# Performance work log

Measured on AMD Instinct MI355X. Metric: run time of the kernel, lower is better.

The kernel has to match this reference:

```python
import jax, jax.numpy as jnp
import numpy as np

B, D1, SN, NF = 32, 49, 32, 16          # batch, n_sais, sqrt_n, n_filters
D_MODEL, HEADS = SN * SN * NF, 16        # 16384, 16
DEPTH = D_MODEL // HEADS                 # 1024
C_IN = 16


def setup_inputs() -> dict:
    key = jax.random.key(0)
    ks = jax.random.split(key, 11)
    mk = lambda k, shape, scale=1.0: jax.random.normal(k, shape, dtype=jnp.float32) * scale
    w_scale = 1.0 / np.sqrt(C_IN)
    return {
        "v": mk(ks[0], (B, D1, SN, SN, C_IN)),
        "k": mk(ks[1], (B, D1, SN, SN, C_IN)),
        "q": mk(ks[2], (B, D1, SN, SN, C_IN)),
        # 1x1x1 Conv3D == pointwise channel matmul: weight [C_in, n_filters] + bias
        "Wq": mk(ks[3], (C_IN, NF), w_scale), "bq": jnp.zeros((NF,), jnp.float32),
        "Wk": mk(ks[4], (C_IN, NF), w_scale), "bk": jnp.zeros((NF,), jnp.float32),
        "Wv": mk(ks[5], (C_IN, NF), w_scale), "bv": jnp.zeros((NF,), jnp.float32),
        "Wo": mk(ks[6], (NF, NF), w_scale),   "bo": jnp.zeros((NF,), jnp.float32),
    }


def _pointwise(x, W, b):
    # Conv3D(kernel=1, padding='same') over [B, d1, h, w, c]
    return jnp.einsum('bdhwc,cf->bdhwf', x, W) + b


def reference(v, k, q, Wq, bq, Wk, bk, Wv, bv, Wo, bo):
    b = q.shape[0]
    # projections (1x1x1 conv3d), then flatten spatial+channel into d_model
    def proj_heads(x, W, bias):
        y = _pointwise(x, W, bias).reshape(b, D1, D_MODEL)       # reshape2d
        y = y.reshape(b, D1, HEADS, DEPTH)                        # split_heads
        return y.transpose(0, 2, 1, 3)                            # [b, h, d1, depth]
    qh = proj_heads(q, Wq, bq)
    kh = proj_heads(k, Wk, bk)
    vh = proj_heads(v, Wv, bv)
    # scaled dot-product attention over the 49 SAI tokens
    scale = 1.0 / jnp.sqrt(jnp.float32(DEPTH))
    scores = jnp.einsum('bhqd,bhkd->bhqk', qh, kh) * scale        # [b, h, 49, 49]
    attn = jax.nn.softmax(scores, axis=-1)
    ctx = jnp.einsum('bhqk,bhkd->bhqd', attn, vh)                 # [b, h, 49, depth]
    ctx = ctx.transpose(0, 2, 1, 3).reshape(b, D1, D_MODEL)       # concat heads
    ctx = ctx.reshape(b, D1, SN, SN, NF)                          # reshape4d
    out = _pointwise(ctx, Wo, bo)                                 # wout conv3d 1x1x1
    return out, attn
```

## Files before the change

### kernel.cpp

```cpp
#include <hip/hip_runtime.h>
#include <hip/hip_bf16.h>


#define NT 49
#define TOKS 16384
#define HSL 1024
#define SLOT 3200
#define ZSWZ(n) (((((n) & 7) ^ (((n) >> 3) & 7))) << 4)

typedef __attribute__((ext_vector_type(8))) short bf16x8;
typedef __attribute__((ext_vector_type(4))) float f32x4;

__device__ __forceinline__ ushort f2bf(float f) {
    union { float f; unsigned u; } v; v.f = f;
    return (ushort)((v.u + 0x7fffu + ((v.u >> 16) & 1u)) >> 16);
}
__device__ __forceinline__ unsigned pk2(float f0, float f1) {
    return (unsigned)f2bf(f0) | ((unsigned)f2bf(f1) << 16);
}
__device__ __forceinline__ float4 f4mul(float s, float4 w) {
    return make_float4(s*w.x, s*w.y, s*w.z, s*w.w);
}
__device__ __forceinline__ float4 f4fma(float s, float4 w, float4 a) {
    a.x = fmaf(s, w.x, a.x); a.y = fmaf(s, w.y, a.y);
    a.z = fmaf(s, w.z, a.z); a.w = fmaf(s, w.w, a.w);
    return a;
}
__device__ __forceinline__ float red4s(float v) {
    v += __shfl_xor(v, 1); v += __shfl_xor(v, 2); return v;
}
__device__ __forceinline__ float4 red4v(float4 v) {
    return make_float4(red4s(v.x), red4s(v.y), red4s(v.z), red4s(v.w));
}

#define W_DECL(mb) \
    const float4 W00 = *(const float4*)((mb)+ 0), W01 = *(const float4*)((mb)+ 4), \
                 W02 = *(const float4*)((mb)+ 8), W03 = *(const float4*)((mb)+12), \
                 W10 = *(const float4*)((mb)+16), W11 = *(const float4*)((mb)+20), \
                 W12 = *(const float4*)((mb)+24), W13 = *(const float4*)((mb)+28), \
                 W20 = *(const float4*)((mb)+32), W21 = *(const float4*)((mb)+36), \
                 W22 = *(const float4*)((mb)+40), W23 = *(const float4*)((mb)+44), \
                 W30 = *(const float4*)((mb)+48), W31 = *(const float4*)((mb)+52), \
                 W32 = *(const float4*)((mb)+56), W33 = *(const float4*)((mb)+60)

#define PROJ_BFLY(a, y0, y1, y2, y3) \
    float4 y0 = f4mul((a).x, W00); y0 = f4fma((a).y, W10, y0); \
    y0 = f4fma((a).z, W20, y0);    y0 = f4fma((a).w, W30, y0); \
    float4 y1 = f4mul((a).x, W01); y1 = f4fma((a).y, W11, y1); \
    y1 = f4fma((a).z, W21, y1);    y1 = f4fma((a).w, W31, y1); \
    float4 y2 = f4mul((a).x, W02); y2 = f4fma((a).y, W12, y2); \
    y2 = f4fma((a).z, W22, y2);    y2 = f4fma((a).w, W32, y2); \
    float4 y3 = f4mul((a).x, W03); y3 = f4fma((a).y, W13, y3); \
    y3 = f4fma((a).z, W23, y3);    y3 = f4fma((a).w, W33, y3); \
    y0 = red4v(y0); y1 = red4v(y1); y2 = red4v(y2); y3 = red4v(y3)

template<int SPLIT, int LOG2S>
__global__ __launch_bounds__(256, 2) void k_scores(
    const float* __restrict__ qin, const float* __restrict__ kin,
    const float* __restrict__ Wq, const float* __restrict__ bq,
    const float* __restrict__ Wk, float* __restrict__ ws1)
{
    __shared__ ushort bufA[64*128];
    __shared__ ushort bufB[64*128];
    __shared__ float  Msh[256];
    __shared__ float  wkbqSh[16];
    __shared__ float  gSh[64];

    const int tid  = threadIdx.x;
    const int lane = tid & 63;
    const int wv   = tid >> 6;
    const int s    = blockIdx.x & (SPLIT - 1);
    const int h    = (blockIdx.x >> LOG2S) & 15;
    const int b    = blockIdx.x >> (LOG2S + 4);

    const float* qbase = qin + (size_t)b*NT*TOKS + h*HSL + s*(1024/SPLIT);
    const float* kbase = kin + (size_t)b*NT*TOKS + h*HSL + s*(1024/SPLIT);

    {
        unsigned* z0 = (unsigned*)bufA; unsigned* z1 = (unsigned*)bufB;
        for (int i = tid; i < 4096; i += 256) { z0[i] = 0u; z1[i] = 0u; }
        const int c1 = tid >> 4, c2 = tid & 15;
        float m = 0.f;
        #pragma unroll
        for (int f = 0; f < 16; ++f) m += Wq[c1*16+f] * Wk[c2*16+f];
        Msh[tid] = m;
        if (tid < 16) {
            float wb = 0.f;
            #pragma unroll
            for (int g = 0; g < 16; ++g) wb += Wk[tid*16+g] * bq[g];
            wkbqSh[tid] = wb;
        }
        if (tid < 64) gSh[tid] = 0.f;
    }
    __syncthreads();

    const float* mb = Msh + (lane & 3)*64;
    W_DECL(mb);

    const int f4 = tid & 31;
    const int t0 = tid >> 5;
    const int r  = f4 & 3;

    f32x4 accS[4];
    #pragma unroll
    for (int nt = 0; nt < 4; ++nt) accS[nt] = (f32x4){0.f,0.f,0.f,0.f};

    for (int kc = 0; kc < 8/SPLIT; ++kc) {
        const float* qc = qbase + kc*128 + f4*4;
        const float* kp = kbase + kc*128 + f4*4;
        float4 qv[7], kv[7];
        #pragma unroll
        for (int i = 0; i < 7; ++i) {
            const int t  = t0 + 8*i;
            const int tc = t < 48 ? t : 48;
            qv[i] = *(const float4*)(qc + (size_t)tc*TOKS);
            kv[i] = *(const float4*)(kp + (size_t)tc*TOKS);
        }
        #pragma unroll
        for (int i = 0; i < 7; ++i) {
            const int t = t0 + 8*i;
            if (t >= NT) {
                qv[i] = make_float4(0.f,0.f,0.f,0.f);
                kv[i] = make_float4(0.f,0.f,0.f,0.f);
            }
            PROJ_BFLY(qv[i], y0, y1, y2, y3);
            uint2 w;
            if      (r == 0) { w.x = pk2(y0.x, y0.y); w.y = pk2(y0.z, y0.w); }
            else if (r == 1) { w.x = pk2(y1.x, y1.y); w.y = pk2(y1.z, y1.w); }
            else if (r == 2) { w.x = pk2(y2.x, y2.y); w.y = pk2(y2.z, y2.w); }
            else             { w.x = pk2(y3.x, y3.y); w.y = pk2(y3.z, y3.w); }
            const int addrA = (t*256 + (f4 >> 2)*32 + r*8) ^ ((t & 7) << 4);
            *(uint2*)((char*)bufA + addrA) = w;
            uint2 wk2; wk2.x = pk2(kv[i].x, kv[i].y); wk2.y = pk2(kv[i].z, kv[i].w);
            const int addrB = (t*256 + f4*8) ^ ((t & 7) << 4);
            *(uint2*)((char*)bufB + addrB) = wk2;
            const float* wb = wkbqSh + r*4;
            const float pg = kv[i].x*wb[0] + kv[i].y*wb[1] + kv[i].z*wb[2] + kv[i].w*wb[3];
            if (pg != 0.f) atomicAdd(&gSh[t], pg);
        }
        __syncthreads();
        #pragma unroll
        for (int ks = 0; ks < 4; ++ks) {
            const int ra  = wv*16 + (lane & 15);
            const int abo = (ra*256 + (ks*32 + (lane >> 4)*8)*2) ^ ((ra & 7) << 4);
            const bf16x8 af = *(const bf16x8*)((const char*)bufA + abo);
            #pragma unroll
            for (int nt = 0; nt < 4; ++nt) {
                const int rb  = nt*16 + (lane & 15);
                const int bbo = (rb*256 + (ks*32 + (lane >> 4)*8)*2) ^ ((rb & 7) << 4);
                const bf16x8 bf = *(const bf16x8*)((const char*)bufB + bbo);
                accS[nt] = __builtin_amdgcn_mfma_f32_16x16x32_bf16(af, bf, accS[nt], 0, 0, 0);
            }
        }
        __syncthreads();
    }

    float* slot = ws1 + (size_t)blockIdx.x * SLOT;
    #pragma unroll
    for (int nt = 0; nt < 4; ++nt) {
        const int col = nt*16 + (lane & 15);
        #pragma unroll
        for (int rr = 0; rr < 4; ++rr) {
            const int row = wv*16 + (lane >> 4)*4 + rr;
            if (row < NT) slot[row*64 + col] = accS[nt][rr];
        }
    }
    if (tid < 64) slot[3136 + tid] = gSh[tid];
}

template<int SPLIT>
__global__ __launch_bounds__(256, 2) void k_softmax(
    const float* __restrict__ ws1, float* __restrict__ attnp,
    ushort* __restrict__ ws2)
{
    __shared__ float sS[NT*69];
    __shared__ float sG[64];
    const int tid = threadIdx.x;
    const float* base = ws1 + (size_t)blockIdx.x * SPLIT * SLOT;

    for (int p = tid; p < 784; p += 256) {
        const int row = p >> 4, c4 = (p & 15) * 4;
        float4 acc = *(const float4*)(base + row*64 + c4);
        #pragma unroll
        for (int s = 1; s < SPLIT; ++s) {
            const float4 a = *(const float4*)(base + s*SLOT + row*64 + c4);
            acc.x += a.x; acc.y += a.y; acc.z += a.z; acc.w += a.w;
        }
        sS[row*69 + c4 + 0] = acc.x;
        sS[row*69 + c4 + 1] = acc.y;
        sS[row*69 + c4 + 2] = acc.z;
        sS[row*69 + c4 + 3] = acc.w;
    }
    if (tid < 64) {
        float g = base[3136 + tid];
        #pragma unroll
        for (int s = 1; s < SPLIT; ++s) g += base[s*SLOT + 3136 + tid];
        sG[tid] = g;
    }
    __syncthreads();

    if (tid < NT) {
        float mx = -1e30f;
        for (int j = 0; j < NT; ++j) {
            const float v = (sS[tid*69 + j] + sG[j]) * 0.03125f;
            sS[tid*69 + j] = v;
            mx = fmaxf(mx, v);
        }
        float ssum = 0.f;
        for (int j = 0; j < NT; ++j) {
            const float e = __expf(sS[tid*69 + j] - mx);
            sS[tid*69 + j] = e; ssum += e;
        }
        const float inv = 1.0f / ssum;
        for (int j = 0; j < NT; ++j) sS[tid*69 + j] *= inv;
    }
    __syncthreads();

    float* ab = attnp + (size_t)blockIdx.x * (NT*NT);
    for (int p = tid; p < NT*NT; p += 256) {
        const int t = p / NT, j = p - t*NT;
        ab[p] = sS[t*69 + j];
    }
    ushort* w2 = ws2 + (size_t)blockIdx.x * 4096;
    for (int p = tid; p < 4096; p += 256) {
        const int t = p >> 6, j = p & 63;
        const float v = (t < NT && j < NT) ? sS[t*69 + j] : 0.f;
        w2[p] = f2bf(v);
    }
}

__global__ __launch_bounds__(256, 2) void k_out(
    const float* __restrict__ vin,
    const float* __restrict__ Wv, const float* __restrict__ bv,
    const float* __restrict__ Wo, const float* __restrict__ bo,
    const ushort* __restrict__ ws2, float* __restrict__ out)
{
    __shared__ unsigned Zt[4096];
    __shared__ float WvoSh[256];
    __shared__ float bvoSh[16];

    const int tid  = threadIdx.x;
    const int lane = tid & 63;
    const int wv   = tid >> 6;
    const int kc   = blockIdx.x & 7;
    const int h    = (blockIdx.x >> 3) & 15;
    const int b    = blockIdx.x >> 7;
    const float* vbase = vin + (size_t)b*NT*TOKS + h*HSL;

    {
        const int c1 = tid >> 4, c2 = tid & 15;
        float wvo = 0.f;
        #pragma unroll
        for (int f = 0; f < 16; ++f) wvo += Wv[c1*16+f] * Wo[f*16+c2];
        WvoSh[tid] = wvo;
        if (tid < 16) {
            float s2 = 0.f;
            #pragma unroll
            for (int g = 0; g < 16; ++g) s2 += bv[g]*Wo[g*16+tid];
            bvoSh[tid] = s2 + bo[tid];
        }
        for (int i = tid; i < 1024; i += 256) {
            const int n = i >> 3, pr = 24 + (i & 7);
            if (pr >= 25)
                *(unsigned*)((char*)Zt + ((n*128 + pr*4) ^ ZSWZ(n))) = 0u;
        }
    }
    __syncthreads();

    const ushort* w2 = ws2 + ((size_t)(blockIdx.x >> 3)) * 4096;
    const int ra = wv*16 + (lane & 15);
    const bf16x8 af0 = *(const bf16x8*)(w2 + ra*64 +      (lane >> 4)*8);
    const bf16x8 af1 = *(const bf16x8*)(w2 + ra*64 + 32 + (lane >> 4)*8);

    const float* mb = WvoSh + (lane & 3)*64;
    W_DECL(mb);

    const int f4 = tid & 31;
    const int t0 = tid >> 5;
    const int r  = f4 & 3;

    float4 vv[7];
    {
        const float* vc = vbase + kc*128 + f4*4;
        #pragma unroll
        for (int i = 0; i < 7; ++i) {
            const int t  = t0 + 8*i;
            const int tc = t < 48 ? t : 48;
            vv[i] = *(const float4*)(vc + (size_t)tc*TOKS);
        }
    }
    #pragma unroll
    for (int i = 0; i < 7; ++i) {
        const int t = t0 + 8*i;
        if (t >= NT) vv[i] = make_float4(0.f,0.f,0.f,0.f);
        PROJ_BFLY(vv[i], y0, y1, y2, y3);
        float4 sel;
        if      (r == 0) sel = y0;
        else if (r == 1) sel = y1;
        else if (r == 2) sel = y2;
        else             sel = y3;
        float4 po;
        po.x = __shfl_xor(sel.x, 32); po.y = __shfl_xor(sel.y, 32);
        po.z = __shfl_xor(sel.z, 32); po.w = __shfl_xor(sel.w, 32);
        if (lane < 32) {
            const int n0 = (f4 >> 2)*16 + r*4;
            const int pair = wv + 4*i;
            *(unsigned*)((char*)Zt + (((n0+0)*128 + pair*4) ^ ZSWZ(n0+0))) = pk2(sel.x, po.x);
            *(unsigned*)((char*)Zt + (((n0+1)*128 + pair*4) ^ ZSWZ(n0+1))) = pk2(sel.y, po.y);
            *(unsigned*)((char*)Zt + (((n0+2)*128 + pair*4) ^ ZSWZ(n0+2))) = pk2(sel.z, po.z);
            *(unsigned*)((char*)Zt + (((n0+3)*128 + pair*4) ^ ZSWZ(n0+3))) = pk2(sel.w, po.w);
        }
    }
    __syncthreads();

    float* obase = out + (size_t)b*NT*TOKS + h*HSL + kc*128;
    #pragma unroll
    for (int nt2 = 0; nt2 < 8; ++nt2) {
        const int n    = nt2*16 + (lane & 15);
        const int swzn = ZSWZ(n);
        const bf16x8 bf0 = *(const bf16x8*)((const char*)Zt + ((n*128 +      (lane >> 4)*16) ^ swzn));
        const bf16x8 bf1 = *(const bf16x8*)((const char*)Zt + ((n*128 + 64 + (lane >> 4)*16) ^ swzn));
        f32x4 acc = (f32x4){0.f, 0.f, 0.f, 0.f};
        acc = __builtin_amdgcn_mfma_f32_16x16x32_bf16(af0, bf0, acc, 0, 0, 0);
        acc = __builtin_amdgcn_mfma_f32_16x16x32_bf16(af1, bf1, acc, 0, 0, 0);
        const float bias = bvoSh[n & 15];
        #pragma unroll
        for (int r2 = 0; r2 < 4; ++r2) {
            const int row = wv*16 + (lane >> 4)*4 + r2;
            if (row < NT) obase[(size_t)row*TOKS + n] = acc[r2] + bias;
        }
    }
}

extern "C" void kernel_launch(void* const* d_in, const int* in_sizes, int n_in,
                              void* d_out, int out_size, void* d_ws, size_t ws_size,
                              hipStream_t stream) {
    const float* v  = (const float*)d_in[0];
    const float* k  = (const float*)d_in[1];
    const float* q  = (const float*)d_in[2];
    const float* Wq = (const float*)d_in[3];
    const float* bq = (const float*)d_in[4];
    const float* Wk = (const float*)d_in[5];
    const float* bk = (const float*)d_in[6];
    const float* Wv = (const float*)d_in[7];
    const float* bv = (const float*)d_in[8];
    const float* Wo = (const float*)d_in[9];
    const float* bo = (const float*)d_in[10];
    (void)bk; (void)in_sizes; (void)n_in; (void)out_size;

    float* outp  = (float*)d_out;
    float* attnp = outp + (size_t)32 * 49 * 16384;
    float* ws1   = (float*)d_ws;

    const size_t need4 = (size_t)2048*SLOT*4 + (size_t)512*4096*2;
    if (ws_size >= need4) {
        ushort* ws2 = (ushort*)(ws1 + (size_t)2048*SLOT);
        k_scores<4,2><<<dim3(2048), dim3(256), 0, stream>>>(q, k, Wq, bq, Wk, ws1);
        k_softmax<4> <<<dim3(512),  dim3(256), 0, stream>>>(ws1, attnp, ws2);
        k_out        <<<dim3(4096), dim3(256), 0, stream>>>(v, Wv, bv, Wo, bo, ws2, outp);
    } else {
        ushort* ws2 = (ushort*)(ws1 + (size_t)1024*SLOT);
        k_scores<2,1><<<dim3(1024), dim3(256), 0, stream>>>(q, k, Wq, bq, Wk, ws1);
        k_softmax<2> <<<dim3(512),  dim3(256), 0, stream>>>(ws1, attnp, ws2);
        k_out        <<<dim3(4096), dim3(256), 0, stream>>>(v, Wv, bv, Wo, bo, ws2, outp);
    }
}
```

Baseline: 152.5 us.

## Prefetch next q/k chunk into registers, hoist loads, use hardware bf16 pack

The first kernel now issues global loads for the next q/k chunk while the current chunk is projected, stored to LDS and fed to MFMA, so load latency overlaps compute. The first chunk's loads, and in the output kernel the v and ws2 loads, are moved ahead of the shared-memory setup and weight precompute. The software round-to-nearest bf16 packing is replaced by the v_cvt_pk_bf16_f32 instruction. This costs more live registers, which may hurt occupancy under the 2-block launch bounds.

Result: slower. 158.8 us (+4.1%).

```diff
diff --git a/kernel.cpp b/kernel.cpp
--- a/kernel.cpp
+++ b/kernel.cpp
@@ -15,8 +15,10 @@
     union { float f; unsigned u; } v; v.f = f;
     return (ushort)((v.u + 0x7fffu + ((v.u >> 16) & 1u)) >> 16);
 }
-__device__ __forceinline__ unsigned pk2(float f0, float f1) {
-    return (unsigned)f2bf(f0) | ((unsigned)f2bf(f1) << 16);
+__device__ __forceinline__ unsigned pk2(float lo, float hi) {
+    unsigned r;
+    asm("v_cvt_pk_bf16_f32 %0, %1, %2" : "=v"(r) : "v"(lo), "v"(hi));
+    return r;
 }
 __device__ __forceinline__ float4 f4mul(float s, float4 w) {
     return make_float4(s*w.x, s*w.y, s*w.z, s*w.w);
@@ -76,6 +78,23 @@
     const float* qbase = qin + (size_t)b*NT*TOKS + h*HSL + s*(1024/SPLIT);
     const float* kbase = kin + (size_t)b*NT*TOKS + h*HSL + s*(1024/SPLIT);
 
+    const int f4 = tid & 31;
+    const int t0 = tid >> 5;
+    const int r  = f4 & 3;
+
+    float4 qv[7], kv[7];
+    {
+        const float* qc = qbase + f4*4;
+        const float* kp = kbase + f4*4;
+        #pragma unroll
+        for (int i = 0; i < 7; ++i) {
+            const int t  = t0 + 8*i;
+            const int tc = t < 48 ? t : 48;
+            qv[i] = *(const float4*)(qc + (size_t)tc*TOKS);
+            kv[i] = *(const float4*)(kp + (size_t)tc*TOKS);
+        }
+    }
+
     {
         unsigned* z0 = (unsigned*)bufA; unsigned* z1 = (unsigned*)bufB;
         for (int i = tid; i < 4096; i += 256) { z0[i] = 0u; z1[i] = 0u; }
@@ -97,33 +116,28 @@
     const float* mb = Msh + (lane & 3)*64;
     W_DECL(mb);
 
-    const int f4 = tid & 31;
-    const int t0 = tid >> 5;
-    const int r  = f4 & 3;
-
     f32x4 accS[4];
     #pragma unroll
     for (int nt = 0; nt < 4; ++nt) accS[nt] = (f32x4){0.f,0.f,0.f,0.f};
 
-    for (int kc = 0; kc < 8/SPLIT; ++kc) {
-        const float* qc = qbase + kc*128 + f4*4;
-        const float* kp = kbase + kc*128 + f4*4;
-        float4 qv[7], kv[7];
+    constexpr int NC = 8 / SPLIT;
+    for (int kc = 0; kc < NC; ++kc) {
+        const float* qn = qbase + (kc+1)*128 + f4*4;
+        const float* kn = kbase + (kc+1)*128 + f4*4;
         #pragma unroll
         for (int i = 0; i < 7; ++i) {
             const int t  = t0 + 8*i;
             const int tc = t < 48 ? t : 48;
-            qv[i] = *(const float4*)(qc + (size_t)tc*TOKS);
-            kv[i] = *(const float4*)(kp + (size_t)tc*TOKS);
-        }
-        #pragma unroll
-        for (int i = 0; i < 7; ++i) {
-            const int t = t0 + 8*i;
+            float4 xq = qv[i], xk = kv[i];
+            if (kc + 1 < NC) {
+                qv[i] = *(const float4*)(qn + (size_t)tc*TOKS);
+                kv[i] = *(const float4*)(kn + (size_t)tc*TOKS);
+            }
             if (t >= NT) {
-                qv[i] = make_float4(0.f,0.f,0.f,0.f);
-                kv[i] = make_float4(0.f,0.f,0.f,0.f);
+                xq = make_float4(0.f,0.f,0.f,0.f);
+                xk = make_float4(0.f,0.f,0.f,0.f);
             }
-            PROJ_BFLY(qv[i], y0, y1, y2, y3);
+            PROJ_BFLY(xq, y0, y1, y2, y3);
             uint2 w;
             if      (r == 0) { w.x = pk2(y0.x, y0.y); w.y = pk2(y0.z, y0.w); }
             else if (r == 1) { w.x = pk2(y1.x, y1.y); w.y = pk2(y1.z, y1.w); }
@@ -131,11 +145,11 @@
             else             { w.x = pk2(y3.x, y3.y); w.y = pk2(y3.z, y3.w); }
             const int addrA = (t*256 + (f4 >> 2)*32 + r*8) ^ ((t & 7) << 4);
             *(uint2*)((char*)bufA + addrA) = w;
-            uint2 wk2; wk2.x = pk2(kv[i].x, kv[i].y); wk2.y = pk2(kv[i].z, kv[i].w);
+            uint2 wk2; wk2.x = pk2(xk.x, xk.y); wk2.y = pk2(xk.z, xk.w);
             const int addrB = (t*256 + f4*8) ^ ((t & 7) << 4);
             *(uint2*)((char*)bufB + addrB) = wk2;
             const float* wb = wkbqSh + r*4;
-            const float pg = kv[i].x*wb[0] + kv[i].y*wb[1] + kv[i].z*wb[2] + kv[i].w*wb[3];
+            const float pg = xk.x*wb[0] + xk.y*wb[1] + xk.z*wb[2] + xk.w*wb[3];
             if (pg != 0.f) atomicAdd(&gSh[t], pg);
         }
         __syncthreads();
@@ -247,6 +261,25 @@
     const int b    = blockIdx.x >> 7;
     const float* vbase = vin + (size_t)b*NT*TOKS + h*HSL;
 
+    const int f4 = tid & 31;
+    const int t0 = tid >> 5;
+    const int r  = f4 & 3;
+
+    float4 vv[7];
+    {
+        const float* vc = vbase + kc*128 + f4*4;
+        #pragma unroll
+        for (int i = 0; i < 7; ++i) {
+            const int t  = t0 + 8*i;
+            const int tc = t < 48 ? t : 48;
+            vv[i] = *(const float4*)(vc + (size_t)tc*TOKS);
+        }
+    }
+    const ushort* w2 = ws2 + ((size_t)(blockIdx.x >> 3)) * 4096;
+    const int ra = wv*16 + (lane & 15);
+    const bf16x8 af0 = *(const bf16x8*)(w2 + ra*64 +      (lane >> 4)*8);
+    const bf16x8 af1 = *(const bf16x8*)(w2 + ra*64 + 32 + (lane >> 4)*8);
+
     {
         const int c1 = tid >> 4, c2 = tid & 15;
         float wvo = 0.f;
@@ -267,28 +300,9 @@
     }
     __syncthreads();
 
-    const ushort* w2 = ws2 + ((size_t)(blockIdx.x >> 3)) * 4096;
-    const int ra = wv*16 + (lane & 15);
-    const bf16x8 af0 = *(const bf16x8*)(w2 + ra*64 +      (lane >> 4)*8);
-    const bf16x8 af1 = *(const bf16x8*)(w2 + ra*64 + 32 + (lane >> 4)*8);
-
     const float* mb = WvoSh + (lane & 3)*64;
     W_DECL(mb);
 
-    const int f4 = tid & 31;
-    const int t0 = tid >> 5;
-    const int r  = f4 & 3;
-
-    float4 vv[7];
-    {
-        const float* vc = vbase + kc*128 + f4*4;
-        #pragma unroll
-        for (int i = 0; i < 7; ++i) {
-            const int t  = t0 + 8*i;
-            const int tc = t < 48 ? t : 48;
-            vv[i] = *(const float4*)(vc + (size_t)tc*TOKS);
-        }
-    }
     #pragma unroll
     for (int i = 0; i < 7; ++i) {
         const int t = t0 + 8*i;
```

## Rework per-thread projection mapping and add SPLIT=8 scores path

Applied to the files above, without the earlier changes.

Replaces the butterfly-shuffle projection, where each lane multiplies 4 channels and reduces across lanes, with a layout in which each thread loads all 16 channels of one spatial point and computes 4 output filters by direct dot products, removing cross-lane shuffles. Q and V loads are software-pipelined one token ahead, and K loads for the first chunk are issued before the shared-memory setup. A new SPLIT=8 configuration launches 4096 score blocks when the workspace is large enough, at the cost of more partial slots for softmax to reduce. The final barrier in the chunk loop is skipped on the last iteration.

Measured after the change: 131.2 us. -13.9%, faster.

```diff
diff --git a/kernel.cpp b/kernel.cpp
--- a/kernel.cpp
+++ b/kernel.cpp
@@ -15,22 +15,20 @@
     union { float f; unsigned u; } v; v.f = f;
     return (ushort)((v.u + 0x7fffu + ((v.u >> 16) & 1u)) >> 16);
 }
-__device__ __forceinline__ unsigned pk2(float f0, float f1) {
-    return (unsigned)f2bf(f0) | ((unsigned)f2bf(f1) << 16);
-}
-__device__ __forceinline__ float4 f4mul(float s, float4 w) {
-    return make_float4(s*w.x, s*w.y, s*w.z, s*w.w);
-}
-__device__ __forceinline__ float4 f4fma(float s, float4 w, float4 a) {
-    a.x = fmaf(s, w.x, a.x); a.y = fmaf(s, w.y, a.y);
-    a.z = fmaf(s, w.z, a.z); a.w = fmaf(s, w.w, a.w);
-    return a;
-}
-__device__ __forceinline__ float red4s(float v) {
-    v += __shfl_xor(v, 1); v += __shfl_xor(v, 2); return v;
-}
-__device__ __forceinline__ float4 red4v(float4 v) {
-    return make_float4(red4s(v.x), red4s(v.y), red4s(v.z), red4s(v.w));
+__device__ __forceinline__ unsigned pk2(float lo, float hi) {
+    return (unsigned)f2bf(lo) | ((unsigned)f2bf(hi) << 16);
+}
+__device__ __forceinline__ float qdot(float4 x0, float4 x1, float4 x2, float4 x3,
+                                      float4 wa, float4 wb, float4 wc, float4 wd) {
+    float s =      x0.x*wa.x;
+    s = fmaf(x0.y, wa.y, s); s = fmaf(x0.z, wa.z, s); s = fmaf(x0.w, wa.w, s);
+    s = fmaf(x1.x, wb.x, s); s = fmaf(x1.y, wb.y, s); s = fmaf(x1.z, wb.z, s);
+    s = fmaf(x1.w, wb.w, s);
+    s = fmaf(x2.x, wc.x, s); s = fmaf(x2.y, wc.y, s); s = fmaf(x2.z, wc.z, s);
+    s = fmaf(x2.w, wc.w, s);
+    s = fmaf(x3.x, wd.x, s); s = fmaf(x3.y, wd.y, s); s = fmaf(x3.z, wd.z, s);
+    s = fmaf(x3.w, wd.w, s);
+    return s;
 }
 
 #define W_DECL(mb) \
@@ -42,17 +40,6 @@
                  W22 = *(const float4*)((mb)+40), W23 = *(const float4*)((mb)+44), \
                  W30 = *(const float4*)((mb)+48), W31 = *(const float4*)((mb)+52), \
                  W32 = *(const float4*)((mb)+56), W33 = *(const float4*)((mb)+60)
-
-#define PROJ_BFLY(a, y0, y1, y2, y3) \
-    float4 y0 = f4mul((a).x, W00); y0 = f4fma((a).y, W10, y0); \
-    y0 = f4fma((a).z, W20, y0);    y0 = f4fma((a).w, W30, y0); \
-    float4 y1 = f4mul((a).x, W01); y1 = f4fma((a).y, W11, y1); \
-    y1 = f4fma((a).z, W21, y1);    y1 = f4fma((a).w, W31, y1); \
-    float4 y2 = f4mul((a).x, W02); y2 = f4fma((a).y, W12, y2); \
-    y2 = f4fma((a).z, W22, y2);    y2 = f4fma((a).w, W32, y2); \
-    float4 y3 = f4mul((a).x, W03); y3 = f4fma((a).y, W13, y3); \
-    y3 = f4fma((a).z, W23, y3);    y3 = f4fma((a).w, W33, y3); \
-    y0 = red4v(y0); y1 = red4v(y1); y2 = red4v(y2); y3 = red4v(y3)
 
 template<int SPLIT, int LOG2S>
 __global__ __launch_bounds__(256, 2) void k_scores(
@@ -76,14 +63,40 @@
     const float* qbase = qin + (size_t)b*NT*TOKS + h*HSL + s*(1024/SPLIT);
     const float* kbase = kin + (size_t)b*NT*TOKS + h*HSL + s*(1024/SPLIT);
 
+    const int f4 = tid & 31;
+    const int t0 = tid >> 5;
+    const int si = (tid >> 2) & 7;
+    const int rq = tid & 3;
+
+    constexpr int NC = 8 / SPLIT;
+
+    float4 kv[7];
+    {
+        const float* kp = kbase + f4*4;
+        #pragma unroll
+        for (int i = 0; i < 7; ++i) {
+            const int t = t0 + 8*i; const int tc = t < 48 ? t : 48;
+            kv[i] = *(const float4*)(kp + (size_t)tc*TOKS);
+        }
+    }
+    float4 xa0, xa1, xa2, xa3;
+    {
+        const float* qc = qbase + si*16 + (size_t)t0*TOKS;
+        xa0 = *(const float4*)(qc);
+        xa1 = *(const float4*)(qc + 4);
+        xa2 = *(const float4*)(qc + 8);
+        xa3 = *(const float4*)(qc + 12);
+    }
+
     {
         unsigned* z0 = (unsigned*)bufA; unsigned* z1 = (unsigned*)bufB;
-        for (int i = tid; i < 4096; i += 256) { z0[i] = 0u; z1[i] = 0u; }
+        #pragma unroll
+        for (int i = 0; i < 16; ++i) { z0[tid + 256*i] = 0u; z1[tid + 256*i] = 0u; }
         const int c1 = tid >> 4, c2 = tid & 15;
         float m = 0.f;
         #pragma unroll
         for (int f = 0; f < 16; ++f) m += Wq[c1*16+f] * Wk[c2*16+f];
-        Msh[tid] = m;
+        Msh[c2*16 + c1] = m;
         if (tid < 16) {
             float wb = 0.f;
             #pragma unroll
@@ -94,49 +107,58 @@
     }
     __syncthreads();
 
-    const float* mb = Msh + (lane & 3)*64;
-    W_DECL(mb);
-
-    const int f4 = tid & 31;
-    const int t0 = tid >> 5;
-    const int r  = f4 & 3;
+    W_DECL(Msh + rq*64);
 
     f32x4 accS[4];
     #pragma unroll
     for (int nt = 0; nt < 4; ++nt) accS[nt] = (f32x4){0.f,0.f,0.f,0.f};
 
-    for (int kc = 0; kc < 8/SPLIT; ++kc) {
-        const float* qc = qbase + kc*128 + f4*4;
-        const float* kp = kbase + kc*128 + f4*4;
-        float4 qv[7], kv[7];
-        #pragma unroll
-        for (int i = 0; i < 7; ++i) {
-            const int t  = t0 + 8*i;
-            const int tc = t < 48 ? t : 48;
-            qv[i] = *(const float4*)(qc + (size_t)tc*TOKS);
-            kv[i] = *(const float4*)(kp + (size_t)tc*TOKS);
+    for (int kc = 0; kc < NC; ++kc) {
+        if (kc > 0) {
+            const float* kp = kbase + kc*128 + f4*4;
+            #pragma unroll
+            for (int i = 0; i < 7; ++i) {
+                const int t = t0 + 8*i; const int tc = t < 48 ? t : 48;
+                kv[i] = *(const float4*)(kp + (size_t)tc*TOKS);
+            }
+            const float* qc = qbase + kc*128 + si*16 + (size_t)t0*TOKS;
+            xa0 = *(const float4*)(qc);
+            xa1 = *(const float4*)(qc + 4);
+            xa2 = *(const float4*)(qc + 8);
+            xa3 = *(const float4*)(qc + 12);
         }
         #pragma unroll
         for (int i = 0; i < 7; ++i) {
             const int t = t0 + 8*i;
-            if (t >= NT) {
-                qv[i] = make_float4(0.f,0.f,0.f,0.f);
-                kv[i] = make_float4(0.f,0.f,0.f,0.f);
+            float4 xk = kv[i];
+            if (t >= NT) xk = make_float4(0.f,0.f,0.f,0.f);
+            uint2 w; w.x = pk2(xk.x, xk.y); w.y = pk2(xk.z, xk.w);
+            *(uint2*)((char*)bufB + ((t*256 + f4*8) ^ ((t & 7) << 4))) = w;
+            const float* wb = wkbqSh + (f4 & 3)*4;
+            const float pg = xk.x*wb[0] + xk.y*wb[1] + xk.z*wb[2] + xk.w*wb[3];
+            if (pg != 0.f) atomicAdd(&gSh[t], pg);
+        }
+        #pragma unroll
+        for (int i = 0; i < 7; ++i) {
+            float4 xb0 = xa0, xb1 = xa1, xb2 = xa2, xb3 = xa3;
+            if (i < 6) {
+                const int tn = t0 + 8*(i+1); const int tc = tn < 48 ? tn : 48;
+                const float* qc = qbase + kc*128 + si*16 + (size_t)tc*TOKS;
+                xb0 = *(const float4*)(qc);
+                xb1 = *(const float4*)(qc + 4);
+                xb2 = *(const float4*)(qc + 8);
+                xb3 = *(const float4*)(qc + 12);
             }
-            PROJ_BFLY(qv[i], y0, y1, y2, y3);
-            uint2 w;
-            if      (r == 0) { w.x = pk2(y0.x, y0.y); w.y = pk2(y0.z, y0.w); }
-            else if (r == 1) { w.x = pk2(y1.x, y1.y); w.y = pk2(y1.z, y1.w); }
-            else if (r == 2) { w.x = pk2(y2.x, y2.y); w.y = pk2(y2.z, y2.w); }
-            else             { w.x = pk2(y3.x, y3.y); w.y = pk2(y3.z, y3.w); }
-            const int addrA = (t*256 + (f4 >> 2)*32 + r*8) ^ ((t & 7) << 4);
-            *(uint2*)((char*)bufA + addrA) = w;
-            uint2 wk2; wk2.x = pk2(kv[i].x, kv[i].y); wk2.y = pk2(kv[i].z, kv[i].w);
-            const int addrB = (t*256 + f4*8) ^ ((t & 7) << 4);
-            *(uint2*)((char*)bufB + addrB) = wk2;
-            const float* wb = wkbqSh + r*4;
-            const float pg = kv[i].x*wb[0] + kv[i].y*wb[1] + kv[i].z*wb[2] + kv[i].w*wb[3];
-            if (pg != 0.f) atomicAdd(&gSh[t], pg);
+            const int t = t0 + 8*i;
+            if (t < NT) {
+                const float o0 = qdot(xa0,xa1,xa2,xa3, W00,W01,W02,W03);
+                const float o1 = qdot(xa0,xa1,xa2,xa3, W10,W11,W12,W13);
+                const float o2 = qdot(xa0,xa1,xa2,xa3, W20,W21,W22,W23);
+                const float o3 = qdot(xa0,xa1,xa2,xa3, W30,W31,W32,W33);
+                uint2 w; w.x = pk2(o0, o1); w.y = pk2(o2, o3);
+                *(uint2*)((char*)bufA + ((t*256 + si*32 + rq*8) ^ ((t & 7) << 4))) = w;
+            }
+            xa0 = xb0; xa1 = xb1; xa2 = xb2; xa3 = xb3;
         }
         __syncthreads();
         #pragma unroll
@@ -152,7 +174,7 @@
                 accS[nt] = __builtin_amdgcn_mfma_f32_16x16x32_bf16(af, bf, accS[nt], 0, 0, 0);
             }
         }
-        __syncthreads();
+        if (kc + 1 < NC) __syncthreads();
     }
 
     float* slot = ws1 + (size_t)blockIdx.x * SLOT;
@@ -247,69 +269,67 @@
     const int b    = blockIdx.x >> 7;
     const float* vbase = vin + (size_t)b*NT*TOKS + h*HSL;
 
+    const int si = (tid >> 2) & 7;
+    const int rq = tid & 3;
+    const int t0 = tid >> 5;
+
+    const ushort* w2 = ws2 + ((size_t)(blockIdx.x >> 3)) * 4096;
+    const int ra = wv*16 + (lane & 15);
+    const bf16x8 af0 = *(const bf16x8*)(w2 + ra*64 +      (lane >> 4)*8);
+    const bf16x8 af1 = *(const bf16x8*)(w2 + ra*64 + 32 + (lane >> 4)*8);
+    float4 xa0, xa1, xa2, xa3;
+    {
+        const float* vc = vbase + kc*128 + si*16 + (size_t)t0*TOKS;
+        xa0 = *(const float4*)(vc);
+        xa1 = *(const float4*)(vc + 4);
+        xa2 = *(const float4*)(vc + 8);
+        xa3 = *(const float4*)(vc + 12);
+    }
+
     {
         const int c1 = tid >> 4, c2 = tid & 15;
         float wvo = 0.f;
         #pragma unroll
         for (int f = 0; f < 16; ++f) wvo += Wv[c1*16+f] * Wo[f*16+c2];
-        WvoSh[tid] = wvo;
+        WvoSh[c2*16 + c1] = wvo;
         if (tid < 16) {
             float s2 = 0.f;
             #pragma unroll
             for (int g = 0; g < 16; ++g) s2 += bv[g]*Wo[g*16+tid];
             bvoSh[tid] = s2 + bo[tid];
         }
-        for (int i = tid; i < 1024; i += 256) {
-            const int n = i >> 3, pr = 24 + (i & 7);
-            if (pr >= 25)
-                *(unsigned*)((char*)Zt + ((n*128 + pr*4) ^ ZSWZ(n))) = 0u;
-        }
-    }
-    __syncthreads();
-
-    const ushort* w2 = ws2 + ((size_t)(blockIdx.x >> 3)) * 4096;
-    const int ra = wv*16 + (lane & 15);
-    const bf16x8 af0 = *(const bf16x8*)(w2 + ra*64 +      (lane >> 4)*8);
-    const bf16x8 af1 = *(const bf16x8*)(w2 + ra*64 + 32 + (lane >> 4)*8);
-
-    const float* mb = WvoSh + (lane & 3)*64;
-    W_DECL(mb);
-
-    const int f4 = tid & 31;
-    const int t0 = tid >> 5;
-    const int r  = f4 & 3;
-
-    float4 vv[7];
-    {
-        const float* vc = vbase + kc*128 + f4*4;
-        #pragma unroll
-        for (int i = 0; i < 7; ++i) {
-            const int t  = t0 + 8*i;
-            const int tc = t < 48 ? t : 48;
-            vv[i] = *(const float4*)(vc + (size_t)tc*TOKS);
-        }
-    }
+        #pragma unroll
+        for (int i = 0; i < 16; ++i) Zt[tid + 256*i] = 0u;
+    }
+    __syncthreads();
+
+    W_DECL(WvoSh + rq*64);
+
     #pragma unroll
     for (int i = 0; i < 7; ++i) {
+        float4 xb0 = xa0, xb1 = xa1, xb2 = xa2, xb3 = xa3;
+        if (i < 6) {
+            const int tn = t0 + 8*(i+1); const int tc = tn < 48 ? tn : 48;
+            const float* vc = vbase + kc*128 + si*16 + (size_t)tc*TOKS;
+            xb0 = *(const float4*)(vc);
+            xb1 = *(const float4*)(vc + 4);
+            xb2 = *(const float4*)(vc + 8);
+            xb3 = *(const float4*)(vc + 12);
+        }
         const int t = t0 + 8*i;
-        if (t >= NT) vv[i] = make_float4(0.f,0.f,0.f,0.f);
-        PROJ_BFLY(vv[i], y0, y1, y2, y3);
-        float4 sel;
-        if      (r == 0) sel = y0;
-        else if (r == 1) sel = y1;
-        else if (r == 2) sel = y2;
-        else             sel = y3;
-        float4 po;
-        po.x = __shfl_xor(sel.x, 32); po.y = __shfl_xor(sel.y, 32);
-        po.z = __shfl_xor(sel.z, 32); po.w = __shfl_xor(sel.w, 32);
-        if (lane < 32) {
-            const int n0 = (f4 >> 2)*16 + r*4;
-            const int pair = wv + 4*i;
-            *(unsigned*)((char*)Zt + (((n0+0)*128 + pair*4) ^ ZSWZ(n0+0))) = pk2(sel.x, po.x);
-            *(unsigned*)((char*)Zt + (((n0+1)*128 + pair*4) ^ ZSWZ(n0+1))) = pk2(sel.y, po.y);
-            *(unsigned*)((char*)Zt + (((n0+2)*128 + pair*4) ^ ZSWZ(n0+2))) = pk2(sel.z, po.z);
-            *(unsigned*)((char*)Zt + (((n0+3)*128 + pair*4) ^ ZSWZ(n0+3))) = pk2(sel.w, po.w);
-        }
+        if (t < NT) {
+            const float o0 = qdot(xa0,xa1,xa2,xa3, W00,W01,W02,W03);
+            const float o1 = qdot(xa0,xa1,xa2,xa3, W10,W11,W12,W13);
+            const float o2 = qdot(xa0,xa1,xa2,xa3, W20,W21,W22,W23);
+            const float o3 = qdot(xa0,xa1,xa2,xa3, W30,W31,W32,W33);
+            const int n0 = si*16 + rq*4;
+            const int pb = (t >> 1)*4, hb = (t & 1)*2;
+            *(ushort*)((char*)Zt + ((((n0+0)*128 + pb) ^ ZSWZ(n0+0)) + hb)) = f2bf(o0);
+            *(ushort*)((char*)Zt + ((((n0+1)*128 + pb) ^ ZSWZ(n0+1)) + hb)) = f2bf(o1);
+            *(ushort*)((char*)Zt + ((((n0+2)*128 + pb) ^ ZSWZ(n0+2)) + hb)) = f2bf(o2);
+            *(ushort*)((char*)Zt + ((((n0+3)*128 + pb) ^ ZSWZ(n0+3)) + hb)) = f2bf(o3);
+        }
+        xa0 = xb0; xa1 = xb1; xa2 = xb2; xa3 = xb3;
     }
     __syncthreads();
 
@@ -352,8 +372,14 @@
     float* attnp = outp + (size_t)32 * 49 * 16384;
     float* ws1   = (float*)d_ws;
 
+    const size_t need8 = (size_t)4096*SLOT*4 + (size_t)512*4096*2;
     const size_t need4 = (size_t)2048*SLOT*4 + (size_t)512*4096*2;
-    if (ws_size >= need4) {
+    if (ws_size >= need8) {
+        ushort* ws2 = (ushort*)(ws1 + (size_t)4096*SLOT);
+        k_scores<8,3><<<dim3(4096), dim3(256), 0, stream>>>(q, k, Wq, bq, Wk, ws1);
+        k_softmax<8> <<<dim3(512),  dim3(256), 0, stream>>>(ws1, attnp, ws2);
+        k_out        <<<dim3(4096), dim3(256), 0, stream>>>(v, Wv, bv, Wo, bo, ws2, outp);
+    } else if (ws_size >= need4) {
         ushort* ws2 = (ushort*)(ws1 + (size_t)2048*SLOT);
         k_scores<4,2><<<dim3(2048), dim3(256), 0, stream>>>(q, k, Wq, bq, Wk, ws1);
         k_softmax<4> <<<dim3(512),  dim3(256), 0, stream>>>(ws1, attnp, ws2);
```
